# Optimization experiments

Hardware: AMD Instinct MI355X
Metric: run time of the kernel (lower is better)

Reference implementation:

```python
import jax, jax.numpy as jnp
import numpy as np

EPS = 0.001

def batchnorm(x, gamma, beta):
    # x: [N, C, H, W]; training-mode batch statistics over (N, H, W), biased variance (torch BN)
    mean = jnp.mean(x, axis=(0, 2, 3), keepdims=True)
    var = jnp.mean(jnp.square(x - mean), axis=(0, 2, 3), keepdims=True)
    xn = (x - mean) * jax.lax.rsqrt(var + EPS)
    return xn * gamma[None, :, None, None] + beta[None, :, None, None]

def setup_inputs() -> dict:
    key = jax.random.key(0)
    ks = jax.random.split(key, 6)
    N, C, C2, H, W = 8, 256, 256, 96, 96
    num_heads, key_dim, value_dim = 8, 32, 32
    q_input = jax.random.normal(ks[0], (N, C, H, W), dtype=jnp.float32)
    kv = jax.random.normal(ks[1], (N, C2, H, W), dtype=jnp.float32)
    # 1x1 conv weights as matrices [out, in], kaiming-normal-ish scale
    Wq = jax.random.normal(ks[2], (key_dim * num_heads, C), dtype=jnp.float32) * np.sqrt(2.0 / C)
    Wk = jax.random.normal(ks[3], (key_dim * num_heads, C2), dtype=jnp.float32) * np.sqrt(2.0 / C2)
    Wv = jax.random.normal(ks[4], (value_dim * num_heads, C2), dtype=jnp.float32) * np.sqrt(2.0 / C2)
    Wp = jax.random.normal(ks[5], (C, value_dim * num_heads), dtype=jnp.float32) * np.sqrt(2.0 / (value_dim * num_heads))
    return {
        "q_input": q_input, "kv": kv,
        "Wq": Wq, "Wk": Wk, "Wv": Wv, "Wp": Wp,
        "q_gamma": jnp.ones((C,), jnp.float32), "q_beta": jnp.zeros((C,), jnp.float32),
        "kv_gamma": jnp.ones((C2,), jnp.float32), "kv_beta": jnp.zeros((C2,), jnp.float32),
    }

def reference(q_input, kv, Wq, Wk, Wv, Wp, q_gamma, q_beta, kv_gamma, kv_beta):
    NUM_HEADS, KEY_DIM, VALUE_DIM = 8, 32, 32
    n, C, q_h, q_w = q_input.shape
    _, C2, kv_h, kv_w = kv.shape
    Lq, Lk = q_h * q_w, kv_h * kv_w
    qn = batchnorm(q_input, q_gamma, q_beta)
    kvn = batchnorm(kv, kv_gamma, kv_beta)
    # 1x1 convs == channel matmuls; reshape to [n, heads, dim, L]
    queries = jnp.einsum('oc,nchw->nohw', Wq, qn).reshape(n, NUM_HEADS, KEY_DIM, Lq)
    keys = jnp.einsum('oc,nchw->nohw', Wk, kvn).reshape(n, NUM_HEADS, KEY_DIM, Lk)
    values = jnp.einsum('oc,nchw->nohw', Wv, kvn).reshape(n, NUM_HEADS, VALUE_DIM, Lk)
    key_sm = jax.nn.softmax(keys, axis=-1)        # softmax over kv spatial positions
    query_sm = jax.nn.softmax(queries, axis=2)    # softmax over key_dim channels
    # context[k,v] = sum_l key[k,l] * value[v,l]
    context = jnp.einsum('nhkl,nhvl->nhkv', key_sm, values)
    # attended[v,q] = sum_k context[k,v] * query[k,q]
    attended = jnp.einsum('nhkv,nhkq->nhvq', context, query_sm)
    aggregated = attended.reshape(n, NUM_HEADS * VALUE_DIM, Lq)
    reproj = jnp.einsum('cv,nvq->ncq', Wp, aggregated).reshape(n, C, q_h, q_w)
    return reproj + q_input
```

## Files before the change

### kernel.cpp

```cpp
#include <hip/hip_runtime.h>

#define L 9216
#define CNTF 73728.0f

#define F_DENOM 1024
#define F_CTX 3072
#define F_STATS 68608
#define B_M2 274432u
#define B_QSM 38023168u

#define O_WF 0u
#define O_BIAS 393216u

typedef float floatx4 __attribute__((ext_vector_type(4)));
typedef __bf16 bf16x8 __attribute__((ext_vector_type(8)));

__device__ __forceinline__ unsigned short f2bf(float f){
  return __builtin_bit_cast(unsigned short, (__bf16)f);
}
__device__ __forceinline__ unsigned pack2(float lo, float hi){
  return (unsigned)f2bf(lo) | ((unsigned)f2bf(hi) << 16);
}
__device__ __forceinline__ int swz(int r){ return (r ^ (r >> 4)) & 7; }
__device__ __forceinline__ int sw4(int r){ return (r ^ (r >> 4)) & 15; }

__device__ __forceinline__ void gload16(const void* g, void* l){
  __builtin_amdgcn_global_load_lds(
      (const __attribute__((address_space(1))) unsigned*)g,
      (__attribute__((address_space(3))) unsigned*)l, 16, 0, 0);
}

__global__ __launch_bounds__(256) void k_init(float* __restrict__ ws){
  int i = blockIdx.x * 256 + threadIdx.x;
  if (i < 68608) ws[F_DENOM + i] = 0.0f;
}

__global__ __launch_bounds__(256, 4) void k_stats(const float* __restrict__ q,
                                                  const float* __restrict__ kv,
                                                  float* __restrict__ ws){
  int b = blockIdx.x, t = threadIdx.x;
  int ten = b >> 11;
  int row = b & 2047;
  int c = row & 255;
  const float4* p = (const float4*)((ten ? kv : q) + (size_t)row * L);
  float4 v0 = p[t        ], v1 = p[t +  256], v2 = p[t +  512];
  float4 v3 = p[t +  768 ], v4 = p[t + 1024], v5 = p[t + 1280];
  float4 v6 = p[t + 1536 ], v7 = p[t + 1792], v8 = p[t + 2048];
  float s0 = v0.x+v0.y+v0.z+v0.w, q0 = v0.x*v0.x+v0.y*v0.y+v0.z*v0.z+v0.w*v0.w;
  float s1 = v1.x+v1.y+v1.z+v1.w, q1 = v1.x*v1.x+v1.y*v1.y+v1.z*v1.z+v1.w*v1.w;
  float s2 = v2.x+v2.y+v2.z+v2.w, q2 = v2.x*v2.x+v2.y*v2.y+v2.z*v2.z+v2.w*v2.w;
  s0 += v3.x+v3.y+v3.z+v3.w; q0 += v3.x*v3.x+v3.y*v3.y+v3.z*v3.z+v3.w*v3.w;
  s1 += v4.x+v4.y+v4.z+v4.w; q1 += v4.x*v4.x+v4.y*v4.y+v4.z*v4.z+v4.w*v4.w;
  s2 += v5.x+v5.y+v5.z+v5.w; q2 += v5.x*v5.x+v5.y*v5.y+v5.z*v5.z+v5.w*v5.w;
  s0 += v6.x+v6.y+v6.z+v6.w; q0 += v6.x*v6.x+v6.y*v6.y+v6.z*v6.z+v6.w*v6.w;
  s1 += v7.x+v7.y+v7.z+v7.w; q1 += v7.x*v7.x+v7.y*v7.y+v7.z*v7.z+v7.w*v7.w;
  s2 += v8.x+v8.y+v8.z+v8.w; q2 += v8.x*v8.x+v8.y*v8.y+v8.z*v8.z+v8.w*v8.w;
  float s = s0 + s1 + s2, ss = q0 + q1 + q2;
  #pragma unroll
  for (int off = 1; off < 64; off <<= 1){
    s += __shfl_xor(s, off); ss += __shfl_xor(ss, off);
  }
  __shared__ float r4[2][4];
  int w = t >> 6;
  if ((t & 63) == 0){ r4[0][w] = s; r4[1][w] = ss; }
  __syncthreads();
  if (t == 0){
    s  = r4[0][0]+r4[0][1]+r4[0][2]+r4[0][3];
    ss = r4[1][0]+r4[1][1]+r4[1][2]+r4[1][3];
    atomicAdd(&ws[F_STATS + ten*512 + c], s);
    atomicAdd(&ws[F_STATS + ten*512 + 256 + c], ss);
  }
}

__global__ __launch_bounds__(256) void k_wfold(const float* __restrict__ W0,
    const float* __restrict__ W1, const float* __restrict__ W2,
    const float* __restrict__ ws,
    const float* __restrict__ qg, const float* __restrict__ qb,
    const float* __restrict__ kg, const float* __restrict__ kb,
    char* __restrict__ outa){
  __shared__ float sc[256], sh[256];
  int b = blockIdx.x, r = threadIdx.x;
  int tsel = (b < 2) ? 1 : 0;
  {
    float s  = ws[F_STATS + tsel*512 + r];
    float ssum = ws[F_STATS + tsel*512 + 256 + r];
    float m = s * (1.0f/CNTF);
    float vv = ssum * (1.0f/CNTF) - m*m;
    float g  = tsel ? kg[r] : qg[r];
    float be = tsel ? kb[r] : qb[r];
    float scv = rsqrtf(vv + 1e-3f) * g;
    sc[r] = scv; sh[r] = be - m*scv;
  }
  __syncthreads();
  const float* W = (b == 0) ? W0 : ((b == 1) ? W1 : W2);
  const float* wrow = W + (size_t)r * 256;
  int imgrow, biasidx;
  char* chunk;
  if (b < 2){
    int h = r >> 5;
    imgrow = (h >> 1)*128 + (h & 1)*64 + b*32 + (r & 31);
    biasidx = imgrow;
    chunk = outa + O_WF;
  } else {
    imgrow = r;
    biasidx = 512 + r;
    chunk = outa + O_WF + 262144;
  }
  int opl = imgrow >> 7, rl = imgrow & 127;
  float bias = 0.f;
  for (int kc = 0; kc < 4; ++kc){
    unsigned pk[8][4];
    #pragma unroll
    for (int g = 0; g < 8; ++g){
      float v[8];
      #pragma unroll
      for (int m = 0; m < 8; ++m){
        int k = kc*64 + g*8 + m;
        float w = wrow[k];
        v[m] = w * sc[k];
        bias = fmaf(w, sh[k], bias);
      }
      pk[g][0] = pack2(v[0], v[1]); pk[g][1] = pack2(v[2], v[3]);
      pk[g][2] = pack2(v[4], v[5]); pk[g][3] = pack2(v[6], v[7]);
    }
    #pragma unroll
    for (int g = 0; g < 8; ++g){
      int idx = (opl*4 + kc)*1024 + rl*8 + (g ^ swz(rl));
      *(uint4*)(chunk + (size_t)idx*16) =
          make_uint4(pk[g][0], pk[g][1], pk[g][2], pk[g][3]);
    }
  }
  ((float*)(outa + O_BIAS))[biasidx] = bias;
}

__global__ __launch_bounds__(256, 2) void k_fkv(
    const char* __restrict__ Af, const float* __restrict__ kv,
    const float* __restrict__ bias, float* __restrict__ ws)
{
  __shared__ __align__(16) ushort SH[128*128];
  ushort* As = SH;
  ushort* Bs = SH + 128*64;
  char*   EV = (char*)SH;
  const int t = threadIdx.x;
  const int lane = t & 63, wid = t >> 6;
  const int wr = wid >> 1, wc = wid & 1;
  const int bid = blockIdx.x;
  const int xcd = bid & 7, seq = bid >> 3;
  const int op = seq & 3;
  const int lpi = (seq >> 2) & 3;
  const int gid = xcd * 18 + (seq >> 4);
  const int lpg = gid % 18, n = gid / 18;
  const int l0 = (lpg*4 + lpi) * 128;
  const char* Achunk = Af + (size_t)op * 65536;
  const int cpair = t >> 3, lg = t & 7;
  const int lcol = lane & 15, lhi = lane >> 4;
  const int lrow4 = lhi * 4;

  floatx4 c16[2] = {};
  float dn[2][4] = {};

  floatx4 acc[4][4] = {};
  for (int kc = 0; kc < 4; ++kc){
    {
      const char* src = Achunk + kc*16384 + ((size_t)(wid*4*64 + lane))*16;
      ushort* dst = As + wid*4*512;
      gload16(src,        dst);
      gload16(src + 1024, dst + 512);
      gload16(src + 2048, dst + 1024);
      gload16(src + 3072, dst + 1536);
    }
    unsigned bu[16];
    {
      const float* Xa = kv + ((size_t)(n*256 + kc*64 + 2*cpair))*L + l0 + lg*16;
      const float* Xb = Xa + L;
      #pragma unroll
      for (int q = 0; q < 4; ++q){
        float4 a = ((const float4*)Xa)[q];
        float4 b = ((const float4*)Xb)[q];
        bu[4*q+0] = pack2(a.x, b.x);
        bu[4*q+1] = pack2(a.y, b.y);
        bu[4*q+2] = pack2(a.z, b.z);
        bu[4*q+3] = pack2(a.w, b.w);
      }
    }
    {
      int g = cpair >> 2, d = cpair & 3;
      #pragma unroll
      for (int j = 0; j < 16; ++j){
        int ll = lg*16 + j;
        *(unsigned*)((char*)Bs + ll*128 + ((g ^ swz(ll))*16) + d*4) = bu[j];
      }
    }
    __syncthreads();
    #pragma unroll
    for (int ks = 0; ks < 2; ++ks){
      bf16x8 af[4], bfr[4];
      #pragma unroll
      for (int mf = 0; mf < 4; ++mf){
        int row = wr*64 + mf*16 + lcol;
        int gq = (ks*4 + lhi) ^ swz(row);
        af[mf] = *(const bf16x8*)(As + row*64 + gq*8);
      }
      #pragma unroll
      for (int nf = 0; nf < 4; ++nf){
        int ll = wc*64 + nf*16 + lcol;
        int gq = (ks*4 + lhi) ^ swz(ll);
        bfr[nf] = *(const bf16x8*)(Bs + ll*64 + gq*8);
      }
      #pragma unroll
      for (int mf = 0; mf < 4; ++mf)
        #pragma unroll
        for (int nf = 0; nf < 4; ++nf)
          acc[mf][nf] = __builtin_amdgcn_mfma_f32_16x16x32_bf16(af[mf], bfr[nf], acc[mf][nf], 0, 0, 0);
    }
    __syncthreads();
  }

  #pragma unroll
  for (int mf = 0; mf < 4; ++mf)
    #pragma unroll
    for (int r = 0; r < 4; ++r){
      float bv = bias[op*128 + wr*64 + mf*16 + lrow4 + r];
      if (mf < 2){
        #pragma unroll
        for (int nf = 0; nf < 4; ++nf)
          acc[mf][nf][r] = __expf(acc[mf][nf][r] + bv);
      } else {
        #pragma unroll
        for (int nf = 0; nf < 4; ++nf)
          acc[mf][nf][r] += bv;
      }
    }
  #pragma unroll
  for (int mf = 0; mf < 2; ++mf)
    #pragma unroll
    for (int r = 0; r < 4; ++r){
      float s = acc[mf][0][r] + acc[mf][1][r] + acc[mf][2][r] + acc[mf][3][r];
      s += __shfl_xor(s, 1); s += __shfl_xor(s, 2);
      s += __shfl_xor(s, 4); s += __shfl_xor(s, 8);
      dn[mf][r] += s;
    }
  #pragma unroll
  for (int mf = 0; mf < 4; ++mf)
    #pragma unroll
    for (int nf = 0; nf < 4; ++nf)
      #pragma unroll
      for (int r = 0; r < 4; ++r){
        int row = wr*64 + mf*16 + lrow4 + r;
        int col = wc*64 + nf*16 + lcol;
        int g = (col >> 3) ^ sw4(row);
        *(ushort*)(EV + row*256 + g*16 + (col & 7)*2) = f2bf(acc[mf][nf][r]);
      }
  __syncthreads();
  #pragma unroll
  for (int kk = 0; kk < 4; ++kk){
    int gk = (kk*32 + lhi*8) >> 3;
    bf16x8 aE0, aE1, bV;
    {
      int row = wr*64 + lcol;
      aE0 = *(const bf16x8*)(EV + row*256 + ((gk ^ sw4(row))*16));
    }
    {
      int row = wr*64 + 16 + lcol;
      aE1 = *(const bf16x8*)(EV + row*256 + ((gk ^ sw4(row))*16));
    }
    {
      int row = wr*64 + 32 + wc*16 + lcol;
      bV = *(const bf16x8*)(EV + row*256 + ((gk ^ sw4(row))*16));
    }
    c16[0] = __builtin_amdgcn_mfma_f32_16x16x32_bf16(aE0, bV, c16[0], 0, 0, 0);
    c16[1] = __builtin_amdgcn_mfma_f32_16x16x32_bf16(aE1, bV, c16[1], 0, 0, 0);
  }

  float* ctxp = ws + F_CTX + (size_t)((n*8) + op*2 + wr)*1024;
  #pragma unroll
  for (int i0 = 0; i0 < 2; ++i0)
    #pragma unroll
    for (int r = 0; r < 4; ++r)
      atomicAdd(ctxp + (i0*16 + lrow4 + r)*32 + wc*16 + lcol, c16[i0][r]);
  if (lcol == 0){
    float* dnp = ws + F_DENOM + (size_t)((n*8) + op*2 + wr)*32;
    #pragma unroll
    for (int mf = 0; mf < 2; ++mf)
      #pragma unroll
      for (int r = 0; r < 4; ++r)
        atomicAdd(dnp + mf*16 + lrow4 + r, dn[mf][r]);
  }
}

template<int MODE>
__global__ __launch_bounds__(256, 3) void k_gemm(
    const char* __restrict__ Af, size_t a_nstride,
    const void* __restrict__ Bsrc,
    const float* __restrict__ bias,
    void* __restrict__ outp, const float* __restrict__ xres)
{
  __shared__ __align__(16) ushort SH[128*128];
  ushort* As = SH;
  ushort* Bs = SH + 128*64;
  const int t = threadIdx.x;
  const int lane = t & 63, wid = t >> 6;
  const int wr = wid >> 1, wc = wid & 1;
  const int bid = blockIdx.x;
  const int xcd = bid & 7, seq = bid >> 3;
  const int op = seq & 1;
  const int gid = xcd * 72 + (seq >> 1);
  const int lp = gid % 72, n = gid / 72;
  const int l0 = lp * 128, o0 = op * 128;
  const char* Achunk = Af + (size_t)n * a_nstride + (size_t)op * 65536;
  const char* Bn = (const char*)Bsrc + (size_t)n * 4718592;
  const int cpair = t >> 3, lg = t & 7;
  const int lcol = lane & 15, lhi = lane >> 4;
  const int r8 = lane >> 3, s8 = lane & 7;

  floatx4 acc[4][4] = {};

  for (int kc = 0; kc < 4; ++kc) {
    {
      const char* src = Achunk + kc*16384 + ((size_t)(wid*4*64 + lane))*16;
      ushort* dst = As + wid*4*512;
      gload16(src,        dst);
      gload16(src + 1024, dst + 512);
      gload16(src + 2048, dst + 1024);
      gload16(src + 3072, dst + 1536);
    }
    if (MODE == 2) {
      #pragma unroll
      for (int i = 0; i < 4; ++i){
        int rw = wid*32 + i*8 + r8;
        const char* src = Bn + (size_t)(l0 + rw)*512 + kc*128 + ((s8 ^ swz(rw))*16);
        gload16(src, Bs + (wid*32 + i*8)*64);
      }
    } else {
      unsigned bu[16];
      const float* Xa = (const float*)Bsrc + ((size_t)(n*256 + kc*64 + 2*cpair))*L + l0 + lg*16;
      const float* Xb = Xa + L;
      #pragma unroll
      for (int q = 0; q < 4; ++q) {
        float4 a = ((const float4*)Xa)[q];
        float4 b = ((const float4*)Xb)[q];
        bu[4*q+0] = pack2(a.x, b.x);
        bu[4*q+1] = pack2(a.y, b.y);
        bu[4*q+2] = pack2(a.z, b.z);
        bu[4*q+3] = pack2(a.w, b.w);
      }
      int g = cpair >> 2, d = cpair & 3;
      #pragma unroll
      for (int j = 0; j < 16; ++j){
        int ll = lg*16 + j;
        *(unsigned*)((char*)Bs + ll*128 + ((g ^ swz(ll))*16) + d*4) = bu[j];
      }
    }
    __syncthreads();
    #pragma unroll
    for (int ks = 0; ks < 2; ++ks) {
      bf16x8 af[4], bfr[4];
      #pragma unroll
      for (int mf = 0; mf < 4; ++mf) {
        int row = wr*64 + mf*16 + lcol;
        int gq = (ks*4 + lhi) ^ swz(row);
        af[mf] = *(const bf16x8*)(As + row*64 + gq*8);
      }
      #pragma unroll
      for (int nf = 0; nf < 4; ++nf) {
        int ll = wc*64 + nf*16 + lcol;
        int gq = (ks*4 + lhi) ^ swz(ll);
        bfr[nf] = *(const bf16x8*)(Bs + ll*64 + gq*8);
      }
      #pragma unroll
      for (int mf = 0; mf < 4; ++mf)
        #pragma unroll
        for (int nf = 0; nf < 4; ++nf)
          acc[mf][nf] = __builtin_amdgcn_mfma_f32_16x16x32_bf16(af[mf], bfr[nf], acc[mf][nf], 0, 0, 0);
    }
    __syncthreads();
  }

  const int lrow4 = lhi * 4;

  if (MODE == 1) {
    #pragma unroll
    for (int mf = 0; mf < 4; ++mf)
      #pragma unroll
      for (int r = 0; r < 4; ++r) {
        float bv = bias[o0 + wr*64 + mf*16 + lrow4 + r];
        #pragma unroll
        for (int nf = 0; nf < 4; ++nf)
          acc[mf][nf][r] = __expf(acc[mf][nf][r] + bv);
      }
    #pragma unroll
    for (int hg = 0; hg < 2; ++hg) {
      #pragma unroll
      for (int nf = 0; nf < 4; ++nf) {
        float s = 0.f;
        #pragma unroll
        for (int mh = 0; mh < 2; ++mh)
          #pragma unroll
          for (int r = 0; r < 4; ++r)
            s += acc[hg*2+mh][nf][r];
        s += __shfl_xor(s, 16);
        s += __shfl_xor(s, 32);
        float inv = 1.0f / s;
        #pragma unroll
        for (int mh = 0; mh < 2; ++mh)
          #pragma unroll
          for (int r = 0; r < 4; ++r)
            acc[hg*2+mh][nf][r] *= inv;
      }
    }
    ushort* Lst = SH;
    #pragma unroll
    for (int mf = 0; mf < 4; ++mf){
      int ol = wr*64 + mf*16 + lrow4;
      int och = ol >> 3;
      #pragma unroll
      for (int nf = 0; nf < 4; ++nf){
        int ll = wc*64 + nf*16 + lcol;
        unsigned w0 = pack2(acc[mf][nf][0], acc[mf][nf][1]);
        unsigned w1 = pack2(acc[mf][nf][2], acc[mf][nf][3]);
        char* p = (char*)Lst + ll*256 + ((och ^ sw4(ll))*16) + (ol & 7)*2;
        *(unsigned*)p = w0;
        *(unsigned*)(p + 4) = w1;
      }
    }
    __syncthreads();
    char* ob = (char*)outp + (size_t)(n*9216 + l0)*512 + o0*2;
    #pragma unroll
    for (int j = 0; j < 8; ++j){
      int flat = j*256 + t;
      int l = flat >> 4, seg = flat & 15;
      uint4 v = *(const uint4*)((const char*)Lst + l*256 + ((seg ^ sw4(l))*16));
      *(uint4*)(ob + (size_t)l*512 + seg*16) = v;
    }
  }

  if (MODE == 2) {
    float* outf = (float*)outp;
    #pragma unroll
    for (int mf = 0; mf < 4; ++mf)
      #pragma unroll
      for (int r = 0; r < 4; ++r) {
        int orow = o0 + wr*64 + mf*16 + lrow4 + r;
        size_t base = ((size_t)n*256 + orow)*L + l0 + wc*64 + lcol;
        #pragma unroll
        for (int nf = 0; nf < 4; ++nf) {
          size_t gi = base + (size_t)nf*16;
          outf[gi] = acc[mf][nf][r] + xres[gi];
        }
      }
  }
}

__global__ __launch_bounds__(256) void k_m2(const float* __restrict__ Wp,
                                            float* __restrict__ ws)
{
  __shared__ float cn[32][33];
  int t = threadIdx.x, bx = blockIdx.x;
  int n = bx >> 3, h = bx & 7;
  int nh = bx;
  #pragma unroll
  for (int jj = 0; jj < 4; ++jj){
    int i = jj*256 + t;
    int k = i >> 5, v = i & 31;
    cn[k][v] = ws[F_CTX + (size_t)nh*1024 + i] / ws[F_DENOM + nh*32 + k];
  }
  __syncthreads();
  int c = t;
  const float* wrow = Wp + (size_t)c*256 + h*32;
  float w[32];
  #pragma unroll
  for (int v = 0; v < 32; ++v) w[v] = wrow[v];
  float s[32];
  #pragma unroll
  for (int k = 0; k < 32; ++k){
    float a = 0.f;
    #pragma unroll
    for (int v = 0; v < 32; ++v) a = fmaf(w[v], cn[k][v], a);
    s[k] = a;
  }
  char* base = (char*)ws + B_M2 + (size_t)n*131072;
  int opl = c >> 7, rl = c & 127, kc = h >> 1;
  #pragma unroll
  for (int gg = 0; gg < 4; ++gg){
    int g = (h & 1)*4 + gg;
    uint4 u = make_uint4(pack2(s[gg*8+0], s[gg*8+1]), pack2(s[gg*8+2], s[gg*8+3]),
                         pack2(s[gg*8+4], s[gg*8+5]), pack2(s[gg*8+6], s[gg*8+7]));
    *(uint4*)(base + (size_t)((opl*4 + kc)*1024 + rl*8 + (g ^ swz(rl)))*16) = u;
  }
}

extern "C" void kernel_launch(void* const* d_in, const int* in_sizes, int n_in,
                              void* d_out, int out_size, void* d_ws, size_t ws_size,
                              hipStream_t stream)
{
  const float* q_in = (const float*)d_in[0];
  const float* kv   = (const float*)d_in[1];
  const float* Wq   = (const float*)d_in[2];
  const float* Wk   = (const float*)d_in[3];
  const float* Wv   = (const float*)d_in[4];
  const float* Wp   = (const float*)d_in[5];
  const float* qg   = (const float*)d_in[6];
  const float* qb   = (const float*)d_in[7];
  const float* kg   = (const float*)d_in[8];
  const float* kb   = (const float*)d_in[9];
  float* out = (float*)d_out;
  float* wsf = (float*)d_ws;
  char*  outa = (char*)d_out;
  const float* biasf = (const float*)(outa + O_BIAS);

  k_init <<<dim3(268),  dim3(256), 0, stream>>>(wsf);
  k_stats<<<dim3(4096), dim3(256), 0, stream>>>(q_in, kv, wsf);
  k_wfold<<<dim3(3),    dim3(256), 0, stream>>>(Wk, Wv, Wq, wsf, qg, qb, kg, kb, outa);
  k_fkv  <<<dim3(2304), dim3(256), 0, stream>>>(outa + O_WF, kv, biasf, wsf);
  k_m2   <<<dim3(64),   dim3(256), 0, stream>>>(Wp, wsf);
  k_gemm<1><<<dim3(1152), dim3(256), 0, stream>>>(outa + O_WF + 262144, 0, q_in,
      biasf + 512, (char*)d_ws + B_QSM, nullptr);
  k_gemm<2><<<dim3(1152), dim3(256), 0, stream>>>((char*)d_ws + B_M2, 131072,
      (char*)d_ws + B_QSM, nullptr, out, q_in);
}
```

Baseline: 177.7 us.

## Fold init and m2 kernels into neighbours, drop stats atomics, swap fkv MFMA operands

Removes the zero-init kernel by clearing denominators and context inside k_wfold, and stores per-row batchnorm partial sums directly instead of using atomics. The small Wp-context kernel is merged as extra blocks into the first gemm launch. The fkv kernel swaps MFMA operands so the softmax denominator reduction and bf16 stores can be packed, with fewer atomics. This cuts launch count and atomic traffic but places the m2 work in the same grid as the gemm.

```diff
diff --git a/kernel.cpp b/kernel.cpp
--- a/kernel.cpp
+++ b/kernel.cpp
@@ -28,11 +28,6 @@
   __builtin_amdgcn_global_load_lds(
       (const __attribute__((address_space(1))) unsigned*)g,
       (__attribute__((address_space(3))) unsigned*)l, 16, 0, 0);
-}
-
-__global__ __launch_bounds__(256) void k_init(float* __restrict__ ws){
-  int i = blockIdx.x * 256 + threadIdx.x;
-  if (i < 68608) ws[F_DENOM + i] = 0.0f;
 }
 
 __global__ __launch_bounds__(256, 4) void k_stats(const float* __restrict__ q,
@@ -41,7 +36,6 @@
   int b = blockIdx.x, t = threadIdx.x;
   int ten = b >> 11;
   int row = b & 2047;
-  int c = row & 255;
   const float4* p = (const float4*)((ten ? kv : q) + (size_t)row * L);
   float4 v0 = p[t        ], v1 = p[t +  256], v2 = p[t +  512];
   float4 v3 = p[t +  768 ], v4 = p[t + 1024], v5 = p[t + 1280];
@@ -67,14 +61,14 @@
   if (t == 0){
     s  = r4[0][0]+r4[0][1]+r4[0][2]+r4[0][3];
     ss = r4[1][0]+r4[1][1]+r4[1][2]+r4[1][3];
-    atomicAdd(&ws[F_STATS + ten*512 + c], s);
-    atomicAdd(&ws[F_STATS + ten*512 + 256 + c], ss);
+    ws[F_STATS + ten*4096 + row] = s;
+    ws[F_STATS + ten*4096 + 2048 + row] = ss;
   }
 }
 
 __global__ __launch_bounds__(256) void k_wfold(const float* __restrict__ W0,
     const float* __restrict__ W1, const float* __restrict__ W2,
-    const float* __restrict__ ws,
+    float* __restrict__ ws,
     const float* __restrict__ qg, const float* __restrict__ qb,
     const float* __restrict__ kg, const float* __restrict__ kb,
     char* __restrict__ outa){
@@ -82,14 +76,22 @@
   int b = blockIdx.x, r = threadIdx.x;
   int tsel = (b < 2) ? 1 : 0;
   {
-    float s  = ws[F_STATS + tsel*512 + r];
-    float ssum = ws[F_STATS + tsel*512 + 256 + r];
+    float s = 0.f, ssum = 0.f;
+    #pragma unroll
+    for (int n = 0; n < 8; ++n){
+      s    += ws[F_STATS + tsel*4096 + n*256 + r];
+      ssum += ws[F_STATS + tsel*4096 + 2048 + n*256 + r];
+    }
     float m = s * (1.0f/CNTF);
     float vv = ssum * (1.0f/CNTF) - m*m;
     float g  = tsel ? kg[r] : qg[r];
     float be = tsel ? kb[r] : qb[r];
     float scv = rsqrtf(vv + 1e-3f) * g;
     sc[r] = scv; sh[r] = be - m*scv;
+  }
+  for (int j = 0; j < 88; ++j){
+    int i = j*768 + b*256 + r;
+    if (i < 67584) ws[F_DENOM + i] = 0.0f;
   }
   __syncthreads();
   const float* W = (b == 0) ? W0 : ((b == 1) ? W1 : W2);
@@ -156,9 +158,12 @@
   const int lcol = lane & 15, lhi = lane >> 4;
   const int lrow4 = lhi * 4;
 
+  float bv[4];
+  #pragma unroll
+  for (int of = 0; of < 4; ++of)
+    bv[of] = bias[op*128 + wr*64 + of*16 + lcol];
+
   floatx4 c16[2] = {};
-  float dn[2][4] = {};
-
   floatx4 acc[4][4] = {};
   for (int kc = 0; kc < 4; ++kc){
     {
@@ -208,49 +213,48 @@
         bfr[nf] = *(const bf16x8*)(Bs + ll*64 + gq*8);
       }
       #pragma unroll
-      for (int mf = 0; mf < 4; ++mf)
+      for (int lf = 0; lf < 4; ++lf)
         #pragma unroll
-        for (int nf = 0; nf < 4; ++nf)
-          acc[mf][nf] = __builtin_amdgcn_mfma_f32_16x16x32_bf16(af[mf], bfr[nf], acc[mf][nf], 0, 0, 0);
+        for (int of = 0; of < 4; ++of)
+          acc[lf][of] = __builtin_amdgcn_mfma_f32_16x16x32_bf16(bfr[lf], af[of], acc[lf][of], 0, 0, 0);
     }
     __syncthreads();
   }
 
   #pragma unroll
-  for (int mf = 0; mf < 4; ++mf)
-    #pragma unroll
-    for (int r = 0; r < 4; ++r){
-      float bv = bias[op*128 + wr*64 + mf*16 + lrow4 + r];
-      if (mf < 2){
-        #pragma unroll
-        for (int nf = 0; nf < 4; ++nf)
-          acc[mf][nf][r] = __expf(acc[mf][nf][r] + bv);
-      } else {
-        #pragma unroll
-        for (int nf = 0; nf < 4; ++nf)
-          acc[mf][nf][r] += bv;
-      }
-    }
-  #pragma unroll
-  for (int mf = 0; mf < 2; ++mf)
-    #pragma unroll
-    for (int r = 0; r < 4; ++r){
-      float s = acc[mf][0][r] + acc[mf][1][r] + acc[mf][2][r] + acc[mf][3][r];
-      s += __shfl_xor(s, 1); s += __shfl_xor(s, 2);
-      s += __shfl_xor(s, 4); s += __shfl_xor(s, 8);
-      dn[mf][r] += s;
-    }
-  #pragma unroll
-  for (int mf = 0; mf < 4; ++mf)
-    #pragma unroll
-    for (int nf = 0; nf < 4; ++nf)
+  for (int lf = 0; lf < 4; ++lf)
+    #pragma unroll
+    for (int of = 0; of < 4; ++of)
       #pragma unroll
       for (int r = 0; r < 4; ++r){
-        int row = wr*64 + mf*16 + lrow4 + r;
-        int col = wc*64 + nf*16 + lcol;
-        int g = (col >> 3) ^ sw4(row);
-        *(ushort*)(EV + row*256 + g*16 + (col & 7)*2) = f2bf(acc[mf][nf][r]);
-      }
+        if (of < 2) acc[lf][of][r] = __expf(acc[lf][of][r] + bv[of]);
+        else        acc[lf][of][r] += bv[of];
+      }
+  #pragma unroll
+  for (int of = 0; of < 2; ++of){
+    float s = 0.f;
+    #pragma unroll
+    for (int lf = 0; lf < 4; ++lf)
+      #pragma unroll
+      for (int r = 0; r < 4; ++r)
+        s += acc[lf][of][r];
+    s += __shfl_xor(s, 16);
+    s += __shfl_xor(s, 32);
+    if (lhi == 0)
+      atomicAdd(ws + F_DENOM + (size_t)((n*8) + op*2 + wr)*32 + of*16 + lcol, s);
+  }
+  #pragma unroll
+  for (int of = 0; of < 4; ++of){
+    int row = wr*64 + of*16 + lcol;
+    #pragma unroll
+    for (int lf = 0; lf < 4; ++lf){
+      int col = wc*64 + lf*16 + lrow4;
+      int g = (col >> 3) ^ sw4(row);
+      char* p = EV + row*256 + g*16 + (col & 7)*2;
+      *(unsigned*)p       = pack2(acc[lf][of][0], acc[lf][of][1]);
+      *(unsigned*)(p + 4) = pack2(acc[lf][of][2], acc[lf][of][3]);
+    }
+  }
   __syncthreads();
   #pragma unroll
   for (int kk = 0; kk < 4; ++kk){
@@ -278,14 +282,6 @@
     #pragma unroll
     for (int r = 0; r < 4; ++r)
       atomicAdd(ctxp + (i0*16 + lrow4 + r)*32 + wc*16 + lcol, c16[i0][r]);
-  if (lcol == 0){
-    float* dnp = ws + F_DENOM + (size_t)((n*8) + op*2 + wr)*32;
-    #pragma unroll
-    for (int mf = 0; mf < 2; ++mf)
-      #pragma unroll
-      for (int r = 0; r < 4; ++r)
-        atomicAdd(dnp + mf*16 + lrow4 + r, dn[mf][r]);
-  }
 }
 
 template<int MODE>
@@ -293,15 +289,53 @@
     const char* __restrict__ Af, size_t a_nstride,
     const void* __restrict__ Bsrc,
     const float* __restrict__ bias,
-    void* __restrict__ outp, const float* __restrict__ xres)
+    void* __restrict__ outp, const float* __restrict__ xres,
+    const float* __restrict__ Wp, float* __restrict__ wsf)
 {
   __shared__ __align__(16) ushort SH[128*128];
   ushort* As = SH;
   ushort* Bs = SH + 128*64;
   const int t = threadIdx.x;
+  const int bid = blockIdx.x;
+
+  if (MODE == 1 && bid >= 1152){
+    float (*cn)[33] = (float(*)[33])SH;
+    int nh = bid - 1152;
+    int n = nh >> 3, h = nh & 7;
+    #pragma unroll
+    for (int jj = 0; jj < 4; ++jj){
+      int i = jj*256 + t;
+      int k = i >> 5, v = i & 31;
+      cn[k][v] = wsf[F_CTX + (size_t)nh*1024 + i] / wsf[F_DENOM + nh*32 + k];
+    }
+    __syncthreads();
+    int c = t;
+    const float* wrow = Wp + (size_t)c*256 + h*32;
+    float w[32];
+    #pragma unroll
+    for (int v = 0; v < 32; ++v) w[v] = wrow[v];
+    float s[32];
+    #pragma unroll
+    for (int k = 0; k < 32; ++k){
+      float a = 0.f;
+      #pragma unroll
+      for (int v = 0; v < 32; ++v) a = fmaf(w[v], cn[k][v], a);
+      s[k] = a;
+    }
+    char* base = (char*)wsf + B_M2 + (size_t)n*131072;
+    int opl = c >> 7, rl = c & 127, kc = h >> 1;
+    #pragma unroll
+    for (int gg = 0; gg < 4; ++gg){
+      int g = (h & 1)*4 + gg;
+      uint4 u = make_uint4(pack2(s[gg*8+0], s[gg*8+1]), pack2(s[gg*8+2], s[gg*8+3]),
+                           pack2(s[gg*8+4], s[gg*8+5]), pack2(s[gg*8+6], s[gg*8+7]));
+      *(uint4*)(base + (size_t)((opl*4 + kc)*1024 + rl*8 + (g ^ swz(rl)))*16) = u;
+    }
+    return;
+  }
+
   const int lane = t & 63, wid = t >> 6;
   const int wr = wid >> 1, wc = wid & 1;
-  const int bid = blockIdx.x;
   const int xcd = bid & 7, seq = bid >> 3;
   const int op = seq & 1;
   const int gid = xcd * 72 + (seq >> 1);
@@ -448,44 +482,6 @@
           outf[gi] = acc[mf][nf][r] + xres[gi];
         }
       }
-  }
-}
-
-__global__ __launch_bounds__(256) void k_m2(const float* __restrict__ Wp,
-                                            float* __restrict__ ws)
-{
-  __shared__ float cn[32][33];
-  int t = threadIdx.x, bx = blockIdx.x;
-  int n = bx >> 3, h = bx & 7;
-  int nh = bx;
-  #pragma unroll
-  for (int jj = 0; jj < 4; ++jj){
-    int i = jj*256 + t;
-    int k = i >> 5, v = i & 31;
-    cn[k][v] = ws[F_CTX + (size_t)nh*1024 + i] / ws[F_DENOM + nh*32 + k];
-  }
-  __syncthreads();
-  int c = t;
-  const float* wrow = Wp + (size_t)c*256 + h*32;
-  float w[32];
-  #pragma unroll
-  for (int v = 0; v < 32; ++v) w[v] = wrow[v];
-  float s[32];
-  #pragma unroll
-  for (int k = 0; k < 32; ++k){
-    float a = 0.f;
-    #pragma unroll
-    for (int v = 0; v < 32; ++v) a = fmaf(w[v], cn[k][v], a);
-    s[k] = a;
-  }
-  char* base = (char*)ws + B_M2 + (size_t)n*131072;
-  int opl = c >> 7, rl = c & 127, kc = h >> 1;
-  #pragma unroll
-  for (int gg = 0; gg < 4; ++gg){
-    int g = (h & 1)*4 + gg;
-    uint4 u = make_uint4(pack2(s[gg*8+0], s[gg*8+1]), pack2(s[gg*8+2], s[gg*8+3]),
-                         pack2(s[gg*8+4], s[gg*8+5]), pack2(s[gg*8+6], s[gg*8+7]));
-    *(uint4*)(base + (size_t)((opl*4 + kc)*1024 + rl*8 + (g ^ swz(rl)))*16) = u;
   }
 }
 
@@ -508,13 +504,11 @@
   char*  outa = (char*)d_out;
   const float* biasf = (const float*)(outa + O_BIAS);
 
-  k_init <<<dim3(268),  dim3(256), 0, stream>>>(wsf);
   k_stats<<<dim3(4096), dim3(256), 0, stream>>>(q_in, kv, wsf);
   k_wfold<<<dim3(3),    dim3(256), 0, stream>>>(Wk, Wv, Wq, wsf, qg, qb, kg, kb, outa);
   k_fkv  <<<dim3(2304), dim3(256), 0, stream>>>(outa + O_WF, kv, biasf, wsf);
-  k_m2   <<<dim3(64),   dim3(256), 0, stream>>>(Wp, wsf);
-  k_gemm<1><<<dim3(1152), dim3(256), 0, stream>>>(outa + O_WF + 262144, 0, q_in,
-      biasf + 512, (char*)d_ws + B_QSM, nullptr);
+  k_gemm<1><<<dim3(1216), dim3(256), 0, stream>>>(outa + O_WF + 262144, 0, q_in,
+      biasf + 512, (char*)d_ws + B_QSM, nullptr, Wp, wsf);
   k_gemm<2><<<dim3(1152), dim3(256), 0, stream>>>((char*)d_ws + B_M2, 131072,
-      (char*)d_ws + B_QSM, nullptr, out, q_in);
-}
+      (char*)d_ws + B_QSM, nullptr, out, q_in, nullptr, wsf);
+}
```

Result: faster. 151.2 us (-14.9%).
